# Kernel optimization log

Measured on AMD Instinct MI355X. Metric: run time of the kernel, lower is better.

Reference implementation:

```python
import jax, jax.numpy as jnp
import numpy as np

B, S, D = 8, 2048, 1024

def setup_inputs() -> dict:
    key = jax.random.key(0)
    ks = jax.random.split(key, 7)
    x = jax.random.normal(ks[0], (B, S, D), dtype=jnp.float32)
    s = 1.0 / np.sqrt(D)
    Wq = jax.random.normal(ks[1], (D, D), dtype=jnp.float32) * s
    bq = jax.random.normal(ks[2], (D,), dtype=jnp.float32) * 0.01
    Wk = jax.random.normal(ks[3], (D, D), dtype=jnp.float32) * s
    bk = jax.random.normal(ks[4], (D,), dtype=jnp.float32) * 0.01
    Wv = jax.random.normal(ks[5], (D, D), dtype=jnp.float32) * s
    bv = jax.random.normal(ks[6], (D,), dtype=jnp.float32) * 0.01
    return {"x": x, "Wq": Wq, "bq": bq, "Wk": Wk, "bk": bk, "Wv": Wv, "bv": bv}

def reference(x, Wq, bq, Wk, bk, Wv, bv):
    # QKV projections: [B,S,D]
    Q = jnp.einsum('bsd,de->bse', x, Wq) + bq
    K = jnp.einsum('bsd,de->bse', x, Wk) + bk
    V = jnp.einsum('bsd,de->bse', x, Wv) + bv
    scale = 1.0 / jnp.sqrt(jnp.asarray(Q.shape[-1], Q.dtype))
    attn = jnp.einsum('bqd,bkd->bqk', Q, K) * scale  # [B,S,S]
    attn = jax.nn.softmax(attn, axis=-1)
    return jnp.einsum('bqk,bkd->bqd', attn, V)
```

## Files before the change

kernel.cpp:

```cpp
#include <hip/hip_runtime.h>
#include <hip/hip_bf16.h>
#include <cstdint>


#define Bb 8
#define Ss 2048
#define Dd 1024

typedef unsigned short ushort_t;
typedef __attribute__((ext_vector_type(8))) short short8;
typedef __attribute__((ext_vector_type(16))) float floatx16;

__device__ inline ushort_t f2bf(float f) {
    unsigned int u = __float_as_uint(f);
    unsigned int r = (u + 0x7fffu + ((u >> 16) & 1u)) >> 16;
    return (ushort_t)r;
}
__device__ inline float bf2f(ushort_t u) {
    return __uint_as_float(((unsigned int)u) << 16);
}

__device__ inline floatx16 mfma32(short8 a, short8 b, floatx16 c) {
    return __builtin_amdgcn_mfma_f32_32x32x16_bf16(a, b, c, 0, 0, 0);
}

__device__ inline void gload_lds16(const void* g, void* l) {
    __builtin_amdgcn_global_load_lds(
        (const __attribute__((address_space(1))) void*)g,
        (__attribute__((address_space(3))) void*)l, 16, 0, 0);
}

__device__ __attribute__((always_inline)) void gemm_core32(
    const ushort_t* __restrict__ A, const ushort_t* __restrict__ B,
    int K, int lda, int ldb, int m0, int n0, int tid,
    ushort_t* As, ushort_t* Bs, floatx16 acc[2][4])
{
    const int lane = tid & 63;
    const int wave = tid >> 6;
    const int nloc = lane & 31;
    const int h    = lane >> 5;
    const int wm   = (wave & 1) * 64;
    const int wn   = (wave >> 1) * 128;

    const int srow = lane >> 3;
    const int cg   = (lane & 7) ^ srow;
    const ushort_t* aBase = A + (size_t)(m0 + wave * 32 + srow) * lda + cg * 8;
    const ushort_t* bBase = B + (size_t)(n0 + wave * 64 + srow) * ldb + cg * 8;

    int rowA[2], rowB[4];
#pragma unroll
    for (int mt = 0; mt < 2; mt++) rowA[mt] = (wm + mt * 32 + nloc) * 64;
#pragma unroll
    for (int nt = 0; nt < 4; nt++) rowB[nt] = (wn + nt * 32 + nloc) * 64;
    const int xr = lane & 7;

    for (int kt = 0; kt < K; kt += 64) {
#pragma unroll
        for (int j = 0; j < 4; j++)
            gload_lds16(aBase + (size_t)j * 8 * lda + kt, &As[(wave * 4 + j) * 512]);
#pragma unroll
        for (int j = 0; j < 8; j++)
            gload_lds16(bBase + (size_t)j * 8 * ldb + kt, &Bs[(wave * 8 + j) * 512]);
        __syncthreads();

#pragma unroll
        for (int step = 0; step < 4; step++) {
            const int pos = (((step * 2 + h) ^ xr) * 8);
            short8 aF[2], bF[4];
#pragma unroll
            for (int mt = 0; mt < 2; mt++)
                aF[mt] = *(const short8*)&As[rowA[mt] + pos];
#pragma unroll
            for (int nt = 0; nt < 4; nt++)
                bF[nt] = *(const short8*)&Bs[rowB[nt] + pos];
#pragma unroll
            for (int mt = 0; mt < 2; mt++)
#pragma unroll
                for (int nt = 0; nt < 4; nt++)
                    acc[mt][nt] = mfma32(aF[mt], bF[nt], acc[mt][nt]);
        }
        __syncthreads();
    }
}

#define CD_ROW(reg, h) (((reg) & 3) + 8 * ((reg) >> 2) + 4 * (h))

template <int EPI>
__global__ __launch_bounds__(256, 2) void gemm_nt(
    const ushort_t* __restrict__ A, const ushort_t* __restrict__ B,
    void* __restrict__ Cv, const float* __restrict__ aux,
    int K, int lda, int ldb, int ldc,
    size_t strideA, size_t strideB, size_t strideC)
{
    const int z = blockIdx.z;
    A += (size_t)z * strideA;
    B += (size_t)z * strideB;
    const int m0 = blockIdx.y * 128;
    const int n0 = blockIdx.x * 256;

    __shared__ __align__(16) ushort_t As[128 * 64];
    __shared__ __align__(16) ushort_t Bs[256 * 64];

    const int tid  = threadIdx.x;
    const int lane = tid & 63;
    const int wave = tid >> 6;
    const int nloc = lane & 31;
    const int h    = lane >> 5;
    const int wm   = (wave & 1) * 64;
    const int wn   = (wave >> 1) * 128;

    floatx16 acc[2][4] = {};
    gemm_core32(A, B, K, lda, ldb, m0, n0, tid, As, Bs, acc);

    if (EPI == 0) {
        ushort_t* Cb = (ushort_t*)Cv;
#pragma unroll
        for (int nt = 0; nt < 4; nt++) {
            const int gc = n0 + wn + nt * 32 + nloc;
            const float bval = aux[gc];
#pragma unroll
            for (int mt = 0; mt < 2; mt++)
#pragma unroll
                for (int reg = 0; reg < 16; reg++) {
                    const int gr = m0 + wm + mt * 32 + CD_ROW(reg, h);
                    Cb[(size_t)gr * ldc + gc] = f2bf(acc[mt][nt][reg] + bval);
                }
        }
    } else {
        float* Cf = (float*)Cv + (size_t)z * strideC;
#pragma unroll
        for (int mt = 0; mt < 2; mt++)
#pragma unroll
            for (int reg = 0; reg < 16; reg++) {
                const int gr = m0 + wm + mt * 32 + CD_ROW(reg, h);
                const float iv = 1.0f / aux[z * Ss + gr];
#pragma unroll
                for (int nt = 0; nt < 4; nt++) {
                    const int gc = n0 + wn + nt * 32 + nloc;
                    Cf[(size_t)gr * ldc + gc] = acc[mt][nt][reg] * iv;
                }
            }
    }
}

__global__ __launch_bounds__(256, 2) void score_vt(
    const ushort_t* __restrict__ QKVb, ushort_t* __restrict__ Pb,
    ushort_t* __restrict__ Vt, float* __restrict__ lsum)
{
    __shared__ __align__(16) ushort_t As[128 * 64];
    __shared__ __align__(16) ushort_t Bs[256 * 64];
    const int bid = blockIdx.x;
    const int tid = threadIdx.x;

    if (bid < 1024) {
        const int nb = bid & 7, mb = (bid >> 3) & 15, z = bid >> 7;
        const int m0 = mb * 128, n0 = nb * 256;
        const ushort_t* A = QKVb + (size_t)z * Ss * 3072;
        const ushort_t* B = A + 1024;

        floatx16 acc[2][4] = {};
        gemm_core32(A, B, Dd, 3072, 3072, m0, n0, tid, As, Bs, acc);

        const int lane = tid & 63, wave = tid >> 6;
        const int nloc = lane & 31, h = lane >> 5;
        const int wm = (wave & 1) * 64, wn = (wave >> 1) * 128;
        ushort_t* Cp = Pb + (size_t)z * Ss * Ss;

        float rs[2][16] = {};
#pragma unroll
        for (int nt = 0; nt < 4; nt++) {
            const int gc = n0 + wn + nt * 32 + nloc;
#pragma unroll
            for (int mt = 0; mt < 2; mt++)
#pragma unroll
                for (int reg = 0; reg < 16; reg++) {
                    const int gr = m0 + wm + mt * 32 + CD_ROW(reg, h);
                    const ushort_t o = f2bf(__expf(acc[mt][nt][reg] * 0.03125f));
                    Cp[(size_t)gr * Ss + gc] = o;
                    rs[mt][reg] += bf2f(o);
                }
        }
#pragma unroll
        for (int mt = 0; mt < 2; mt++)
#pragma unroll
            for (int reg = 0; reg < 16; reg++) {
                float s = rs[mt][reg];
                s += __shfl_xor(s, 1);
                s += __shfl_xor(s, 2);
                s += __shfl_xor(s, 4);
                s += __shfl_xor(s, 8);
                s += __shfl_xor(s, 16);
                rs[mt][reg] = s;
            }
        if (nloc == 0) {
#pragma unroll
            for (int mt = 0; mt < 2; mt++)
#pragma unroll
                for (int reg = 0; reg < 16; reg++) {
                    const int gr = m0 + wm + mt * 32 + CD_ROW(reg, h);
                    atomicAdd(&lsum[z * Ss + gr], rs[mt][reg]);
                }
        }
    } else {
        const int t = bid - 1024;
        const int z = t >> 9, rem = t & 511;
        const int d0 = (rem & 15) * 64, s0 = (rem >> 4) * 64;
        ushort_t (*tile)[72] = (ushort_t(*)[72])As;
        const int rr = tid >> 3;
        const int c8 = (tid & 7) * 8;
#pragma unroll
        for (int i = 0; i < 2; i++) {
            const int s = s0 + rr + i * 32;
            uint4 v = *(const uint4*)&QKVb[((size_t)(z * Ss + s)) * 3072 + 2048 + d0 + c8];
            *(uint4*)&tile[rr + i * 32][c8] = v;
        }
        __syncthreads();
#pragma unroll
        for (int i = 0; i < 2; i++) {
            const int d = rr + i * 32;
            ushort_t u[8];
#pragma unroll
            for (int j = 0; j < 8; j++) u[j] = tile[c8 + j][d];
            *(uint4*)&Vt[(size_t)z * Dd * Ss + (size_t)(d0 + d) * Ss + s0 + c8] =
                *(const uint4*)u;
        }
    }
}

__global__ __launch_bounds__(256) void prep(
    const float* __restrict__ x,
    const float* __restrict__ W0, const float* __restrict__ W1,
    const float* __restrict__ W2,
    const float* __restrict__ bq, const float* __restrict__ bk,
    const float* __restrict__ bv,
    ushort_t* __restrict__ xb, ushort_t* __restrict__ Wall,
    float* __restrict__ ball)
{
    const int bid = blockIdx.x;
    const int tid = threadIdx.x;

    if (bid < 8192) {
        const size_t i = (size_t)bid * 256 + tid;
        const float4* p = (const float4*)x + i * 2;
        float4 a = p[0], b = p[1];
        ushort_t u[8];
        u[0]=f2bf(a.x); u[1]=f2bf(a.y); u[2]=f2bf(a.z); u[3]=f2bf(a.w);
        u[4]=f2bf(b.x); u[5]=f2bf(b.y); u[6]=f2bf(b.z); u[7]=f2bf(b.w);
        *(uint4*)(xb + i * 8) = *(const uint4*)u;
    } else if (bid < 8960) {
        const int t = bid - 8192;
        const int z = t >> 8;
        const float* W = (z == 0) ? W0 : (z == 1) ? W1 : W2;
        ushort_t* Wt = Wall + (size_t)z * Dd * Dd;
        __shared__ float tt[64][65];
        const int n0 = ((t >> 4) & 15) * 64, k0 = (t & 15) * 64;
        const int r  = tid >> 4;
        const int c4 = (tid & 15) * 4;
#pragma unroll
        for (int i = 0; i < 4; i++) {
            float4 v = *(const float4*)&W[(size_t)(k0 + r + i * 16) * Dd + n0 + c4];
            tt[r + i * 16][c4 + 0] = v.x;
            tt[r + i * 16][c4 + 1] = v.y;
            tt[r + i * 16][c4 + 2] = v.z;
            tt[r + i * 16][c4 + 3] = v.w;
        }
        __syncthreads();
#pragma unroll
        for (int i = 0; i < 4; i++) {
            const int rn = r + i * 16;
            ushort_t u[4];
#pragma unroll
            for (int j = 0; j < 4; j++) u[j] = f2bf(tt[c4 + j][rn]);
            *(uint2*)&Wt[(size_t)(n0 + rn) * Dd + k0 + c4] = *(const uint2*)u;
        }
    } else {
#pragma unroll
        for (int j = 0; j < 12; j++) {
            const int idx = j * 256 + tid;
            float v = (idx < 1024) ? bq[idx]
                    : (idx < 2048) ? bk[idx - 1024] : bv[idx - 2048];
            ball[idx] = v;
        }
    }
}

extern "C" void kernel_launch(void* const* d_in, const int* in_sizes, int n_in,
                              void* d_out, int out_size, void* d_ws, size_t ws_size,
                              hipStream_t stream)
{
    const float* x  = (const float*)d_in[0];
    const float* Wq = (const float*)d_in[1];
    const float* bq = (const float*)d_in[2];
    const float* Wk = (const float*)d_in[3];
    const float* bk = (const float*)d_in[4];
    const float* Wv = (const float*)d_in[5];
    const float* bv = (const float*)d_in[6];
    float* out = (float*)d_out;

    char* ws = (char*)d_ws;
    const size_t MB = 1u << 20;
    ushort_t* xb   = (ushort_t*)(ws);
    ushort_t* Vt   = (ushort_t*)(ws);
    ushort_t* QKVb = (ushort_t*)(ws + 32 * MB);
    ushort_t* Pb   = (ushort_t*)(ws + 128 * MB);
    float*    lsum = (float*)(ws + 192 * MB);
    ushort_t* Wall = (ushort_t*)d_out;
    float*    ball = (float*)((char*)d_out + 6 * MB);

    prep<<<8961, 256, 0, stream>>>(x, Wq, Wk, Wv, bq, bk, bv, xb, Wall, ball);

    dim3 g1(3072 / 256, (Bb * Ss) / 128, 1);
    gemm_nt<0><<<g1, 256, 0, stream>>>(xb, Wall, QKVb, ball,
                                       Dd, Dd, Dd, 3072, 0, 0, 0);

    hipMemsetAsync(lsum, 0, (size_t)Bb * Ss * sizeof(float), stream);
    score_vt<<<5120, 256, 0, stream>>>(QKVb, Pb, Vt, lsum);

    dim3 g3(Dd / 256, Ss / 128, Bb);
    gemm_nt<3><<<g3, 256, 0, stream>>>(Pb, Vt, out, lsum,
                                       Ss, Ss, Ss, Dd,
                                       (size_t)Ss * Ss, (size_t)Dd * Ss,
                                       (size_t)Ss * Dd);
}
```

Baseline: 398.0 us.

## Add row-dependent LDS swizzle in GEMM core and fold lsum zeroing into prep

```diff
diff --git a/kernel.cpp b/kernel.cpp
--- a/kernel.cpp
+++ b/kernel.cpp
@@ -43,36 +43,53 @@
     const int wn   = (wave >> 1) * 128;
 
     const int srow = lane >> 3;
-    const int cg   = (lane & 7) ^ srow;
-    const ushort_t* aBase = A + (size_t)(m0 + wave * 32 + srow) * lda + cg * 8;
-    const ushort_t* bBase = B + (size_t)(n0 + wave * 64 + srow) * ldb + cg * 8;
-
-    int rowA[2], rowB[4];
-#pragma unroll
-    for (int mt = 0; mt < 2; mt++) rowA[mt] = (wm + mt * 32 + nloc) * 64;
-#pragma unroll
-    for (int nt = 0; nt < 4; nt++) rowB[nt] = (wn + nt * 32 + nloc) * 64;
-    const int xr = lane & 7;
+    const int xr   = lane & 7;
+
+    const ushort_t* aPtr[4];
+    const ushort_t* bPtr[8];
+#pragma unroll
+    for (int j = 0; j < 4; j++) {
+        const int cg = xr ^ srow ^ ((wave * 4 + j) & 7);
+        aPtr[j] = A + (size_t)(m0 + wave * 32 + j * 8 + srow) * lda + cg * 8;
+    }
+#pragma unroll
+    for (int j = 0; j < 8; j++) {
+        const int cg = xr ^ srow ^ j;
+        bPtr[j] = B + (size_t)(n0 + wave * 64 + j * 8 + srow) * ldb + cg * 8;
+    }
+
+    int rowA[2], swA[2], rowB[4], swB[4];
+    const int a = nloc & 7, b = nloc >> 3;
+#pragma unroll
+    for (int mt = 0; mt < 2; mt++) {
+        rowA[mt] = (wm + mt * 32 + nloc) * 64;
+        swA[mt]  = a ^ ((4 * mt + b) & 7);
+    }
+#pragma unroll
+    for (int nt = 0; nt < 4; nt++) {
+        rowB[nt] = (wn + nt * 32 + nloc) * 64;
+        swB[nt]  = a ^ ((4 * nt + b) & 7);
+    }
 
     for (int kt = 0; kt < K; kt += 64) {
 #pragma unroll
         for (int j = 0; j < 4; j++)
-            gload_lds16(aBase + (size_t)j * 8 * lda + kt, &As[(wave * 4 + j) * 512]);
+            gload_lds16(aPtr[j] + kt, &As[(wave * 4 + j) * 512]);
 #pragma unroll
         for (int j = 0; j < 8; j++)
-            gload_lds16(bBase + (size_t)j * 8 * ldb + kt, &Bs[(wave * 8 + j) * 512]);
+            gload_lds16(bPtr[j] + kt, &Bs[(wave * 8 + j) * 512]);
         __syncthreads();
 
 #pragma unroll
         for (int step = 0; step < 4; step++) {
-            const int pos = (((step * 2 + h) ^ xr) * 8);
+            const int gk = step * 2 + h;
             short8 aF[2], bF[4];
 #pragma unroll
             for (int mt = 0; mt < 2; mt++)
-                aF[mt] = *(const short8*)&As[rowA[mt] + pos];
+                aF[mt] = *(const short8*)&As[rowA[mt] + ((gk ^ swA[mt]) << 3)];
 #pragma unroll
             for (int nt = 0; nt < 4; nt++)
-                bF[nt] = *(const short8*)&Bs[rowB[nt] + pos];
+                bF[nt] = *(const short8*)&Bs[rowB[nt] + ((gk ^ swB[nt]) << 3)];
 #pragma unroll
             for (int mt = 0; mt < 2; mt++)
 #pragma unroll
@@ -234,7 +251,7 @@
     const float* __restrict__ bq, const float* __restrict__ bk,
     const float* __restrict__ bv,
     ushort_t* __restrict__ xb, ushort_t* __restrict__ Wall,
-    float* __restrict__ ball)
+    float* __restrict__ ball, float* __restrict__ lsum)
 {
     const int bid = blockIdx.x;
     const int tid = threadIdx.x;
@@ -273,7 +290,7 @@
             for (int j = 0; j < 4; j++) u[j] = f2bf(tt[c4 + j][rn]);
             *(uint2*)&Wt[(size_t)(n0 + rn) * Dd + k0 + c4] = *(const uint2*)u;
         }
-    } else {
+    } else if (bid == 8960) {
 #pragma unroll
         for (int j = 0; j < 12; j++) {
             const int idx = j * 256 + tid;
@@ -281,6 +298,9 @@
                     : (idx < 2048) ? bk[idx - 1024] : bv[idx - 2048];
             ball[idx] = v;
         }
+    } else {
+        const int i = (bid - 8961) * 1024 + tid * 4;
+        *(float4*)&lsum[i] = float4{0.f, 0.f, 0.f, 0.f};
     }
 }
 
@@ -307,13 +327,12 @@
     ushort_t* Wall = (ushort_t*)d_out;
     float*    ball = (float*)((char*)d_out + 6 * MB);
 
-    prep<<<8961, 256, 0, stream>>>(x, Wq, Wk, Wv, bq, bk, bv, xb, Wall, ball);
+    prep<<<8977, 256, 0, stream>>>(x, Wq, Wk, Wv, bq, bk, bv, xb, Wall, ball, lsum);
 
     dim3 g1(3072 / 256, (Bb * Ss) / 128, 1);
     gemm_nt<0><<<g1, 256, 0, stream>>>(xb, Wall, QKVb, ball,
                                        Dd, Dd, Dd, 3072, 0, 0, 0);
 
-    hipMemsetAsync(lsum, 0, (size_t)Bb * Ss * sizeof(float), stream);
     score_vt<<<5120, 256, 0, stream>>>(QKVb, Pb, Vt, lsum);
 
     dim3 g3(Dd / 256, Ss / 128, Bb);
```

Result: no change. 400.9 us (+0.7%).
